# Optimization experiments

Hardware: AMD Instinct MI355X
Metric: run time of the kernel (lower is better)

Reference implementation:

```python
import jax, jax.numpy as jnp
import numpy as np

N = 50000
E = 400000
D = 128

def _linear(v, W, b):
    return v @ W + b

def setup_inputs() -> dict:
    key = jax.random.key(0)
    ks = jax.random.split(key, 24)
    inp = {
        'h': jax.random.normal(ks[0], (N, D), jnp.float32),
        'x': jax.random.normal(ks[1], (N, 3), jnp.float32),
        'src': jax.random.randint(ks[2], (E,), 0, N, jnp.int32),
        'dst': jax.random.randint(ks[3], (E,), 0, N, jnp.int32),
        'distances': jax.random.uniform(ks[4], (E,), jnp.float32),
        'bpp_bias': jax.random.uniform(ks[5], (E,), jnp.float32),
        'msa_bias': jax.random.uniform(ks[6], (E,), jnp.float32),
        'chem_bias': jax.random.uniform(ks[7], (E,), jnp.float32),
        'relative_offset': jax.random.normal(ks[8], (E,), jnp.float32),
        'chain_break_mask': jax.random.uniform(ks[9], (E,), jnp.float32),
    }
    s = 0.05
    # weights stored [in, out] (transpose of torch Linear)
    inp['msg_W1'] = jax.random.normal(ks[10], (2 * D + 6, D), jnp.float32) * s
    inp['msg_b1'] = jnp.zeros((D,), jnp.float32)
    inp['msg_W2'] = jax.random.normal(ks[11], (D, D), jnp.float32) * s
    inp['msg_b2'] = jnp.zeros((D,), jnp.float32)
    inp['h_W1'] = jax.random.normal(ks[12], (2 * D, D), jnp.float32) * s
    inp['h_b1'] = jnp.zeros((D,), jnp.float32)
    inp['h_W2'] = jax.random.normal(ks[13], (D, D), jnp.float32) * s
    inp['h_b2'] = jnp.zeros((D,), jnp.float32)
    inp['c_W1'] = jax.random.normal(ks[14], (D, D), jnp.float32) * s
    inp['c_b1'] = jnp.zeros((D,), jnp.float32)
    inp['c_W2'] = jax.random.normal(ks[15], (D, 1), jnp.float32) * s
    inp['c_b2'] = jnp.zeros((1,), jnp.float32)
    return inp

def reference(h, x, src, dst, distances, bpp_bias, msa_bias, chem_bias,
              relative_offset, chain_break_mask,
              msg_W1, msg_b1, msg_W2, msg_b2,
              h_W1, h_b1, h_W2, h_b2,
              c_W1, c_b1, c_W2, c_b2):
    n = h.shape[0]
    h_src = h[src]                      # [E, D]
    h_dst = h[dst]                      # [E, D]
    diff = x[src] - x[dst]              # [E, 3]
    dist2 = (distances * distances)[:, None]
    feat = jnp.concatenate([
        h_src, h_dst, dist2,
        bpp_bias[:, None], msa_bias[:, None], chem_bias[:, None],
        relative_offset[:, None], chain_break_mask[:, None]], axis=-1)  # [E, 2D+6]
    m_ij = jax.nn.silu(_linear(jax.nn.silu(_linear(feat, msg_W1, msg_b1)), msg_W2, msg_b2))  # [E, D]
    counts = jax.ops.segment_sum(jnp.ones((src.shape[0],), h.dtype), src, num_segments=n)[:, None]  # [N,1]
    denom = jnp.maximum(counts, 1.0)
    m_i = jax.ops.segment_sum(m_ij, src, num_segments=n) / denom      # [N, D]
    h_out = h + _linear(jax.nn.silu(_linear(jnp.concatenate([h, m_i], -1), h_W1, h_b1)), h_W2, h_b2)
    coef = jnp.tanh(_linear(jax.nn.silu(_linear(m_ij, c_W1, c_b1)), c_W2, c_b2))  # [E, 1]
    delta = jax.ops.segment_sum(diff * coef, src, num_segments=n) / denom          # [N, 3]
    x_out = x + delta
    return h_out, x_out
```

## Files before the change

### kernel.cpp

```cpp
#include <hip/hip_runtime.h>
#include <hip/hip_bf16.h>

typedef short bf16x8 __attribute__((ext_vector_type(8)));
typedef float f32x16 __attribute__((ext_vector_type(16)));
typedef int   i32x4v __attribute__((ext_vector_type(4)));
typedef unsigned u32;

#define MFMA32(a,b,c) __builtin_amdgcn_mfma_f32_32x32x16_bf16((a),(b),(c),0,0,0)

__device__ __forceinline__ u32 pkbf(float x, float y) {
  union { u32 u; __hip_bfloat16 h[2]; } t;
  t.h[0] = __float2bfloat16(x);
  t.h[1] = __float2bfloat16(y);
  return t.u;
}
__device__ __forceinline__ float bf2f(u32 lo16) {
  union { u32 u; float f; } t; t.u = lo16 << 16; return t.f;
}
__device__ __forceinline__ float silu_f(float v) { return v / (1.f + __expf(-v)); }
__device__ __forceinline__ float tanh_f(float v) {
  float e = __expf(2.f * fabsf(v));
  float t = 1.f - 2.f / (e + 1.f);
  return copysignf(t, v);
}

template<int NT>
__device__ __forceinline__ void stage_w128t(const float* __restrict__ W, short* wA, int tid) {
  for (int p = tid; p < 8192; p += NT) {
    int j = p & 127;
    int k = (p >> 7) << 1;
    u32 u = pkbf(W[k * 128 + j], W[k * 128 + 128 + j]);
    int off = j * 256 + (((k >> 3) ^ (j & 15)) << 4) + ((k & 7) << 1);
    *(u32*)((char*)wA + off) = u;
  }
}
__device__ __forceinline__ bf16x8 ldsA(const short* wA, int j, int kbase) {
  int off = j * 256 + (((kbase >> 3) ^ (j & 15)) << 4);
  return __builtin_bit_cast(bf16x8, *(const i32x4v*)((const char*)wA + off));
}

__device__ __forceinline__ void row_chunks(u32 p0, u32 p1, u32 p2, u32 p3,
                                           u32 p4, u32 p5, u32 p6, u32 p7,
                                           int hi, char* rowptr, int jm) {
  u32 x0 = (u32)__shfl_xor((int)(hi ? p0 : p4), 32);
  u32 x1 = (u32)__shfl_xor((int)(hi ? p1 : p5), 32);
  u32 x2 = (u32)__shfl_xor((int)(hi ? p2 : p6), 32);
  u32 x3 = (u32)__shfl_xor((int)(hi ? p3 : p7), 32);
  i32x4v c0, c1;
  if (hi) {
    c0[0] = (int)x0; c0[1] = (int)x1; c0[2] = (int)p4; c0[3] = (int)p5;
    c1[0] = (int)x2; c1[1] = (int)x3; c1[2] = (int)p6; c1[3] = (int)p7;
  } else {
    c0[0] = (int)p0; c0[1] = (int)p1; c0[2] = (int)x0; c0[3] = (int)x1;
    c1[0] = (int)p2; c1[1] = (int)p3; c1[2] = (int)x2; c1[3] = (int)x3;
  }
  __builtin_nontemporal_store(c0, (i32x4v*)(rowptr + jm * 64 + hi * 32));
  __builtin_nontemporal_store(c1, (i32x4v*)(rowptr + jm * 64 + hi * 32 + 16));
}

__device__ __forceinline__ void trans_store1(const f32x16& a, const float* bias, int hi,
                                             char* rowptr, bool va, int jm) {
  float v[16];
  #pragma unroll
  for (int r = 0; r < 16; ++r) {
    int rowloc = (r & 3) + 8 * (r >> 2) + 4 * hi;
    v[r] = silu_f(a[r] + bias[jm * 32 + rowloc]);
  }
  u32 p0 = pkbf(v[0], v[1]),  p1 = pkbf(v[2], v[3]);
  u32 p2 = pkbf(v[4], v[5]),  p3 = pkbf(v[6], v[7]);
  u32 p4 = pkbf(v[8], v[9]),  p5 = pkbf(v[10], v[11]);
  u32 p6 = pkbf(v[12], v[13]), p7 = pkbf(v[14], v[15]);
  if (va) row_chunks(p0, p1, p2, p3, p4, p5, p6, p7, hi, rowptr, jm);
}

__device__ __forceinline__ void trans_frag1(const f32x16& a, const float* bias, int hi,
                                            i32x4v* fr, char* rowptr, bool va, int jm) {
  float v[16];
  #pragma unroll
  for (int r = 0; r < 16; ++r) {
    int rowloc = (r & 3) + 8 * (r >> 2) + 4 * hi;
    v[r] = silu_f(a[r] + bias[jm * 32 + rowloc]);
  }
  u32 p0 = pkbf(v[0], v[1]),  p1 = pkbf(v[2], v[3]);
  u32 p2 = pkbf(v[4], v[5]),  p3 = pkbf(v[6], v[7]);
  u32 p4 = pkbf(v[8], v[9]),  p5 = pkbf(v[10], v[11]);
  u32 p6 = pkbf(v[12], v[13]), p7 = pkbf(v[14], v[15]);
  {
    u32 g1 = (u32)__shfl_xor((int)(hi ? p0 : p2), 32);
    u32 g2 = (u32)__shfl_xor((int)(hi ? p1 : p3), 32);
    i32x4v w;
    w[0] = hi ? (int)g1 : (int)p0;
    w[1] = hi ? (int)g2 : (int)p1;
    w[2] = hi ? (int)p2 : (int)g1;
    w[3] = hi ? (int)p3 : (int)g2;
    fr[jm * 2] = w;
    u32 g1b = (u32)__shfl_xor((int)(hi ? p4 : p6), 32);
    u32 g2b = (u32)__shfl_xor((int)(hi ? p5 : p7), 32);
    i32x4v w2;
    w2[0] = hi ? (int)g1b : (int)p4;
    w2[1] = hi ? (int)g2b : (int)p5;
    w2[2] = hi ? (int)p6 : (int)g1b;
    w2[3] = hi ? (int)p7 : (int)g2b;
    fr[jm * 2 + 1] = w2;
  }
  if (va) row_chunks(p0, p1, p2, p3, p4, p5, p6, p7, hi, rowptr, jm);
}


__global__ void kconv(const float* __restrict__ h, char* __restrict__ hbf, int total16) {
  int i = blockIdx.x * 256 + threadIdx.x;
  if (i >= total16) return;
  const float4* h4 = (const float4*)h;
  float4 a = h4[(size_t)i * 2], b = h4[(size_t)i * 2 + 1];
  i32x4v w;
  w[0] = (int)pkbf(a.x, a.y); w[1] = (int)pkbf(a.z, a.w);
  w[2] = (int)pkbf(b.x, b.y); w[3] = (int)pkbf(b.z, b.w);
  *(i32x4v*)(hbf + (size_t)i * 16) = w;
}

__global__ void khist(const int* __restrict__ src, int* __restrict__ cnt, int E) {
  int e = blockIdx.x * 256 + threadIdx.x;
  if (e < E) atomicAdd(&cnt[src[e]], 1);
}

__global__ void kscan1(const int* __restrict__ cnt, int* __restrict__ part,
                       int* __restrict__ bsums, int N) {
  __shared__ int sh[1024];
  int tid = threadIdx.x, i = blockIdx.x * 1024 + tid;
  int v = (i < N) ? cnt[i] : 0;
  sh[tid] = v; __syncthreads();
  for (int off = 1; off < 1024; off <<= 1) {
    int t = (tid >= off) ? sh[tid - off] : 0;
    __syncthreads();
    sh[tid] += t;
    __syncthreads();
  }
  if (i < N) part[i] = sh[tid] - v;
  if (tid == 1023) bsums[blockIdx.x] = sh[1023];
}

__global__ void kscan2(int* __restrict__ bsums, int nb) {
  __shared__ int sh[64];
  int tid = threadIdx.x;
  int v = (tid < nb) ? bsums[tid] : 0;
  sh[tid] = v; __syncthreads();
  for (int off = 1; off < 64; off <<= 1) {
    int t = (tid >= off) ? sh[tid - off] : 0;
    __syncthreads();
    sh[tid] += t;
    __syncthreads();
  }
  if (tid < nb) bsums[tid] = sh[tid] - v;
}

__global__ void kscan3(const int* __restrict__ bsums, int* __restrict__ part,
                       int* __restrict__ head, int N) {
  int i = blockIdx.x * 1024 + threadIdx.x;
  if (i < N) {
    int v = part[i] + bsums[blockIdx.x];
    part[i] = v;
    head[i] = v;
  }
}

__global__ void kscatter(const int* __restrict__ src, const int* __restrict__ dst,
                         const float* __restrict__ dist, const float* __restrict__ bpp,
                         const float* __restrict__ msa, const float* __restrict__ chem,
                         const float* __restrict__ rel, const float* __restrict__ cbm,
                         int* __restrict__ head, int* __restrict__ rec, int E) {
  int e = blockIdx.x * 256 + threadIdx.x;
  if (e >= E) return;
  int s = src[e];
  int p = atomicAdd(&head[s], 1);
  float q = dist[e];
  i32x4v a;
  a[0] = s;
  a[1] = dst[e];
  a[2] = (int)pkbf(q * q, bpp[e]);
  a[3] = (int)pkbf(msa[e], chem[e]);
  *(i32x4v*)(rec + (size_t)p * 8) = a;
  rec[(size_t)p * 8 + 4] = (int)pkbf(rel[e], cbm[e]);
}

__global__ __launch_bounds__(512, 2)
void kedgeA(const char* __restrict__ hbf, const int* __restrict__ rec,
            const float* __restrict__ mW1, const float* __restrict__ mb1,
            char* __restrict__ t1, int E)
{
  __shared__ short wA0[16384], wA1[16384];
  __shared__ short wE[2048];
  __shared__ float sb1[128];

  const int tid = threadIdx.x, wid = tid >> 6, lane = tid & 63;
  const int col = lane & 31, hi = lane >> 5;

  stage_w128t<512>(mW1, wA0, tid);
  stage_w128t<512>(mW1 + 16384, wA1, tid);
  for (int p = tid; p < 2048; p += 512) {
    int j = p >> 4, kk = p & 15;
    float w = (kk < 6) ? mW1[(256 + kk) * 128 + j] : 0.f;
    wE[j * 16 + kk] = (short)(pkbf(w, 0.f) & 0xffffu);
  }
  if (tid < 128) sb1[tid] = mb1[tid];
  __syncthreads();

  const int T = (E + 31) / 32;
  const int stride = gridDim.x * 8;
  int t = blockIdx.x * 8 + wid;
  if (t >= T) return;

  int p = t * 32 + col;
  int pc = p < E ? p : E - 1;
  i32x4v ra = *(const i32x4v*)(rec + (size_t)pc * 8);
  int ev2 = rec[(size_t)pc * 8 + 4];

  while (t < T) {
    bool va = p < E;
    int s = ra[0], d = ra[1];

    i32x4v bs[8], bd[8];
    #pragma unroll
    for (int kc = 0; kc < 8; ++kc)
      bs[kc] = *(const i32x4v*)(hbf + (size_t)s * 256 + kc * 32 + hi * 16);
    #pragma unroll
    for (int kc = 0; kc < 8; ++kc)
      bd[kc] = *(const i32x4v*)(hbf + (size_t)d * 256 + kc * 32 + hi * 16);

    int tn = t + stride;
    int pn = tn * 32 + col;
    int pcn = pn < E ? pn : E - 1;
    i32x4v nra = *(const i32x4v*)(rec + (size_t)pcn * 8);
    int nev2 = rec[(size_t)pcn * 8 + 4];

    char* rowptr = t1 + (size_t)p * 256;
    #pragma unroll
    for (int g = 0; g < 2; ++g) {
      f32x16 acc2[2];
      #pragma unroll
      for (int j2 = 0; j2 < 2; ++j2)
        #pragma unroll
        for (int r = 0; r < 16; ++r) acc2[j2][r] = 0.f;

      #pragma unroll
      for (int kc = 0; kc < 8; ++kc) {
        bf16x8 bb = __builtin_bit_cast(bf16x8, bs[kc]);
        #pragma unroll
        for (int j2 = 0; j2 < 2; ++j2)
          acc2[j2] = MFMA32(ldsA(wA0, (g * 2 + j2) * 32 + col, kc * 16 + hi * 8), bb, acc2[j2]);
      }
      #pragma unroll
      for (int kc = 0; kc < 8; ++kc) {
        bf16x8 bb = __builtin_bit_cast(bf16x8, bd[kc]);
        #pragma unroll
        for (int j2 = 0; j2 < 2; ++j2)
          acc2[j2] = MFMA32(ldsA(wA1, (g * 2 + j2) * 32 + col, kc * 16 + hi * 8), bb, acc2[j2]);
      }
      {
        i32x4v ev;
        ev[0] = hi ? 0 : ra[2];
        ev[1] = hi ? 0 : ra[3];
        ev[2] = hi ? 0 : ev2;
        ev[3] = 0;
        bf16x8 be = __builtin_bit_cast(bf16x8, ev);
        #pragma unroll
        for (int j2 = 0; j2 < 2; ++j2) {
          bf16x8 af = __builtin_bit_cast(bf16x8,
              *(const i32x4v*)((const char*)wE + ((g * 2 + j2) * 32 + col) * 32 + hi * 16));
          acc2[j2] = MFMA32(af, be, acc2[j2]);
        }
      }
      #pragma unroll
      for (int j2 = 0; j2 < 2; ++j2)
        trans_store1(acc2[j2], sb1, hi, rowptr, va, g * 2 + j2);
    }

    t = tn; p = pn; ra = nra; ev2 = nev2;
  }
}

__global__ __launch_bounds__(512, 2)
void kedgeB(char* buf,
            const float* __restrict__ mW2, const float* __restrict__ mb2,
            const float* __restrict__ cW1, const float* __restrict__ cb1,
            const float* __restrict__ cW2v, const float* __restrict__ cb2,
            float* __restrict__ coef, int E)
{
  __shared__ short wA2[16384], wA3[16384];
  __shared__ float sb2[128], scb1[128], scw2[128];
  __shared__ float scb2v[1];

  const int tid = threadIdx.x, wid = tid >> 6, lane = tid & 63;
  const int col = lane & 31, hi = lane >> 5;

  stage_w128t<512>(mW2, wA2, tid);
  stage_w128t<512>(cW1, wA3, tid);
  if (tid < 128) {
    sb2[tid] = mb2[tid]; scb1[tid] = cb1[tid]; scw2[tid] = cW2v[tid];
  }
  if (tid == 0) scb2v[0] = cb2[0];
  __syncthreads();

  const int T = (E + 31) / 32;
  const int stride = gridDim.x * 8;
  for (int t = blockIdx.x * 8 + wid; t < T; t += stride) {
    int p = t * 32 + col;
    bool va = p < E;
    int pc = va ? p : E - 1;

    i32x4v b[8];
    #pragma unroll
    for (int kc = 0; kc < 8; ++kc)
      b[kc] = __builtin_nontemporal_load(
          (const i32x4v*)(buf + (size_t)pc * 256 + kc * 32 + hi * 16));

    char* rowptr = buf + (size_t)p * 256;
    i32x4v fr[8];
    #pragma unroll
    for (int g = 0; g < 2; ++g) {
      f32x16 acc2[2];
      #pragma unroll
      for (int j2 = 0; j2 < 2; ++j2)
        #pragma unroll
        for (int r = 0; r < 16; ++r) acc2[j2][r] = 0.f;
      #pragma unroll
      for (int kc = 0; kc < 8; ++kc) {
        bf16x8 bb = __builtin_bit_cast(bf16x8, b[kc]);
        #pragma unroll
        for (int j2 = 0; j2 < 2; ++j2)
          acc2[j2] = MFMA32(ldsA(wA2, (g * 2 + j2) * 32 + col, kc * 16 + hi * 8), bb, acc2[j2]);
      }
      #pragma unroll
      for (int j2 = 0; j2 < 2; ++j2)
        trans_frag1(acc2[j2], sb2, hi, fr, rowptr, va, g * 2 + j2);
    }

    float part = 0.f;
    #pragma unroll
    for (int g = 0; g < 2; ++g) {
      f32x16 acc2[2];
      #pragma unroll
      for (int j2 = 0; j2 < 2; ++j2)
        #pragma unroll
        for (int r = 0; r < 16; ++r) acc2[j2][r] = 0.f;
      #pragma unroll
      for (int kc = 0; kc < 8; ++kc) {
        bf16x8 bb = __builtin_bit_cast(bf16x8, fr[kc]);
        #pragma unroll
        for (int j2 = 0; j2 < 2; ++j2)
          acc2[j2] = MFMA32(ldsA(wA3, (g * 2 + j2) * 32 + col, kc * 16 + hi * 8), bb, acc2[j2]);
      }
      #pragma unroll
      for (int j2 = 0; j2 < 2; ++j2) {
        int jm = g * 2 + j2;
        #pragma unroll
        for (int r = 0; r < 16; ++r) {
          int rowloc = (r & 3) + 8 * (r >> 2) + 4 * hi;
          part += silu_f(acc2[j2][r] + scb1[jm * 32 + rowloc]) * scw2[jm * 32 + rowloc];
        }
      }
    }
    part += __shfl_xor(part, 32);
    float cf = tanh_f(part + scb2v[0]);
    if (va && hi == 0) coef[p] = cf;
  }
}

__global__ __launch_bounds__(256)
void kagg(const char* __restrict__ m_ij, const int* __restrict__ row_start,
          const int* __restrict__ cnt, char* __restrict__ mibf, int N)
{
  int n = blockIdx.x * 16 + (threadIdx.x >> 4);
  int t = threadIdx.x & 15;
  if (n >= N) return;
  int st = row_start[n], c = cnt[n];
  float a[8] = {0.f, 0.f, 0.f, 0.f, 0.f, 0.f, 0.f, 0.f};
  for (int k = 0; k < c; ++k) {
    i32x4v u = __builtin_nontemporal_load(
        (const i32x4v*)(m_ij + (size_t)(st + k) * 256 + t * 16));
    #pragma unroll
    for (int q = 0; q < 4; ++q) {
      u32 w = (u32)u[q];
      a[q * 2]     += bf2f(w & 0xffffu);
      a[q * 2 + 1] += bf2f(w >> 16);
    }
  }
  float inv = 1.f / fmaxf((float)c, 1.f);
  i32x4v o;
  #pragma unroll
  for (int q = 0; q < 4; ++q) o[q] = (int)pkbf(a[q * 2] * inv, a[q * 2 + 1] * inv);
  *(i32x4v*)(mibf + (size_t)n * 256 + t * 16) = o;
}

__global__ __launch_bounds__(256)
void kaggx(const int* __restrict__ row_start, const int* __restrict__ cnt,
           const float* __restrict__ coef, const int* __restrict__ rec,
           const float* __restrict__ x, float* __restrict__ outX, int N)
{
  int n = blockIdx.x * 256 + threadIdx.x;
  if (n >= N) return;
  int st = row_start[n], c = cnt[n];
  float x0 = x[(size_t)n * 3], x1 = x[(size_t)n * 3 + 1], x2 = x[(size_t)n * 3 + 2];
  float dx = 0.f, dy = 0.f, dz = 0.f;
  for (int k = 0; k < c; ++k) {
    float cf = coef[st + k];
    int dn = rec[(size_t)(st + k) * 8 + 1];
    dx += (x0 - x[(size_t)dn * 3])     * cf;
    dy += (x1 - x[(size_t)dn * 3 + 1]) * cf;
    dz += (x2 - x[(size_t)dn * 3 + 2]) * cf;
  }
  float inv = 1.f / fmaxf((float)c, 1.f);
  outX[(size_t)n * 3]     = x0 + dx * inv;
  outX[(size_t)n * 3 + 1] = x1 + dy * inv;
  outX[(size_t)n * 3 + 2] = x2 + dz * inv;
}

__global__ __launch_bounds__(512, 2)
void knode1(const char* __restrict__ hbf, const char* __restrict__ mibf,
            const float* __restrict__ hW1, const float* __restrict__ hb1,
            char* __restrict__ t1h, int N)
{
  __shared__ short wA0[16384], wA1[16384];
  __shared__ float sb1[128];
  const int tid = threadIdx.x, wid = tid >> 6, lane = tid & 63;
  const int col = lane & 31, hi = lane >> 5;
  stage_w128t<512>(hW1, wA0, tid);
  stage_w128t<512>(hW1 + 16384, wA1, tid);
  if (tid < 128) sb1[tid] = hb1[tid];
  __syncthreads();

  int T = (N + 31) / 32;
  int t = blockIdx.x * 8 + wid;
  if (t >= T) return;
  int n = t * 32 + col;
  bool va = n < N;
  int nc = va ? n : N - 1;

  i32x4v bh[8], bm[8];
  #pragma unroll
  for (int kc = 0; kc < 8; ++kc)
    bh[kc] = *(const i32x4v*)(hbf + (size_t)nc * 256 + kc * 32 + hi * 16);
  #pragma unroll
  for (int kc = 0; kc < 8; ++kc)
    bm[kc] = *(const i32x4v*)(mibf + (size_t)nc * 256 + kc * 32 + hi * 16);

  char* rowptr = t1h + (size_t)n * 256;
  #pragma unroll
  for (int g = 0; g < 2; ++g) {
    f32x16 acc2[2];
    #pragma unroll
    for (int j2 = 0; j2 < 2; ++j2)
      #pragma unroll
      for (int r = 0; r < 16; ++r) acc2[j2][r] = 0.f;
    #pragma unroll
    for (int kc = 0; kc < 8; ++kc) {
      bf16x8 bb = __builtin_bit_cast(bf16x8, bh[kc]);
      #pragma unroll
      for (int j2 = 0; j2 < 2; ++j2)
        acc2[j2] = MFMA32(ldsA(wA0, (g * 2 + j2) * 32 + col, kc * 16 + hi * 8), bb, acc2[j2]);
    }
    #pragma unroll
    for (int kc = 0; kc < 8; ++kc) {
      bf16x8 bb = __builtin_bit_cast(bf16x8, bm[kc]);
      #pragma unroll
      for (int j2 = 0; j2 < 2; ++j2)
        acc2[j2] = MFMA32(ldsA(wA1, (g * 2 + j2) * 32 + col, kc * 16 + hi * 8), bb, acc2[j2]);
    }
    #pragma unroll
    for (int j2 = 0; j2 < 2; ++j2)
      trans_store1(acc2[j2], sb1, hi, rowptr, va, g * 2 + j2);
  }
}

__global__ __launch_bounds__(512, 2)
void knode2(const char* __restrict__ t1h, const float* __restrict__ hW2,
            const float* __restrict__ hb2, const float* __restrict__ h,
            float* __restrict__ outH, int N)
{
  __shared__ short wA0[16384];
  __shared__ float sb2[128];
  const int tid = threadIdx.x, wid = tid >> 6, lane = tid & 63;
  const int col = lane & 31, hi = lane >> 5;
  stage_w128t<512>(hW2, wA0, tid);
  if (tid < 128) sb2[tid] = hb2[tid];
  __syncthreads();

  int T = (N + 31) / 32;
  int t = blockIdx.x * 8 + wid;
  if (t >= T) return;
  int n = t * 32 + col;
  bool va = n < N;
  int nc = va ? n : N - 1;

  i32x4v b[8];
  #pragma unroll
  for (int kc = 0; kc < 8; ++kc)
    b[kc] = __builtin_nontemporal_load(
        (const i32x4v*)(t1h + (size_t)nc * 256 + kc * 32 + hi * 16));

  const float4* h4 = (const float4*)h;
  #pragma unroll
  for (int g = 0; g < 2; ++g) {
    f32x16 acc2[2];
    #pragma unroll
    for (int j2 = 0; j2 < 2; ++j2)
      #pragma unroll
      for (int r = 0; r < 16; ++r) acc2[j2][r] = 0.f;
    #pragma unroll
    for (int kc = 0; kc < 8; ++kc) {
      bf16x8 bb = __builtin_bit_cast(bf16x8, b[kc]);
      #pragma unroll
      for (int j2 = 0; j2 < 2; ++j2)
        acc2[j2] = MFMA32(ldsA(wA0, (g * 2 + j2) * 32 + col, kc * 16 + hi * 8), bb, acc2[j2]);
    }
    #pragma unroll
    for (int j2 = 0; j2 < 2; ++j2) {
      int jm = g * 2 + j2;
      #pragma unroll
      for (int rq = 0; rq < 4; ++rq) {
        int j0 = jm * 32 + rq * 8 + hi * 4;
        float4 hv = h4[(size_t)nc * 32 + (j0 >> 2)];
        float4 o;
        o.x = hv.x + acc2[j2][rq * 4 + 0] + sb2[j0 + 0];
        o.y = hv.y + acc2[j2][rq * 4 + 1] + sb2[j0 + 1];
        o.z = hv.z + acc2[j2][rq * 4 + 2] + sb2[j0 + 2];
        o.w = hv.w + acc2[j2][rq * 4 + 3] + sb2[j0 + 3];
        if (va) ((float4*)outH)[(size_t)nc * 32 + (j0 >> 2)] = o;
      }
    }
  }
}


extern "C" void kernel_launch(void* const* d_in, const int* in_sizes, int n_in,
                              void* d_out, int out_size, void* d_ws, size_t ws_size,
                              hipStream_t stream) {
  const float* h    = (const float*)d_in[0];
  const float* x    = (const float*)d_in[1];
  const int*   src  = (const int*)d_in[2];
  const int*   dst  = (const int*)d_in[3];
  const float* dist = (const float*)d_in[4];
  const float* bpp  = (const float*)d_in[5];
  const float* msa  = (const float*)d_in[6];
  const float* chem = (const float*)d_in[7];
  const float* rel  = (const float*)d_in[8];
  const float* cbm  = (const float*)d_in[9];
  const float* mW1  = (const float*)d_in[10];
  const float* mb1  = (const float*)d_in[11];
  const float* mW2  = (const float*)d_in[12];
  const float* mb2  = (const float*)d_in[13];
  const float* hW1  = (const float*)d_in[14];
  const float* hb1  = (const float*)d_in[15];
  const float* hW2  = (const float*)d_in[16];
  const float* hb2  = (const float*)d_in[17];
  const float* cW1  = (const float*)d_in[18];
  const float* cb1  = (const float*)d_in[19];
  const float* cW2  = (const float*)d_in[20];
  const float* cb2  = (const float*)d_in[21];

  int N = in_sizes[0] / 128;
  int E = in_sizes[2];

  size_t off = 0;
  auto A = [&](size_t b) { size_t o = off; off += (b + 255) & ~(size_t)255; return o; };
  size_t o_cnt  = A((size_t)N * 4);
  size_t o_rs   = A((size_t)N * 4);
  size_t o_head = A((size_t)N * 4);
  size_t o_rec  = A((size_t)E * 32);
  size_t o_coef = A((size_t)E * 4);
  size_t o_bs   = A(1024);
  size_t o_hbf  = A((size_t)N * 256);
  size_t o_mibf = A((size_t)N * 256);
  size_t o_big  = A((size_t)E * 256);

  char* W = (char*)d_ws;
  int*   cnt32 = (int*)(W + o_cnt);
  int*   rs    = (int*)(W + o_rs);
  int*   head  = (int*)(W + o_head);
  int*   rec   = (int*)(W + o_rec);
  float* coef  = (float*)(W + o_coef);
  int*   bsums = (int*)(W + o_bs);
  char*  hbf   = W + o_hbf;
  char*  mibf  = W + o_mibf;
  char*  big   = W + o_big;

  hipMemsetAsync(cnt32, 0, (size_t)N * 4, stream);
  kconv<<<(N * 16 + 255) / 256, 256, 0, stream>>>(h, hbf, N * 16);
  khist<<<(E + 255) / 256, 256, 0, stream>>>(src, cnt32, E);
  int nb = (N + 1023) / 1024;
  kscan1<<<nb, 1024, 0, stream>>>(cnt32, rs, bsums, N);
  kscan2<<<1, 64, 0, stream>>>(bsums, nb);
  kscan3<<<nb, 1024, 0, stream>>>(bsums, rs, head, N);
  kscatter<<<(E + 255) / 256, 256, 0, stream>>>(src, dst, dist, bpp, msa, chem, rel, cbm,
                                                head, rec, E);
  kedgeA<<<512, 512, 0, stream>>>(hbf, rec, mW1, mb1, big, E);
  kedgeB<<<512, 512, 0, stream>>>(big, mW2, mb2, cW1, cb1, cW2, cb2, coef, E);
  kagg<<<(N + 15) / 16, 256, 0, stream>>>(big, rs, cnt32, mibf, N);
  kaggx<<<(N + 255) / 256, 256, 0, stream>>>(rs, cnt32, coef, rec, x,
                                             (float*)d_out + (size_t)N * 128, N);
  int tb = ((N + 31) / 32 + 7) / 8;
  knode1<<<tb, 512, 0, stream>>>(hbf, mibf, hW1, hb1, big, N);
  knode2<<<tb, 512, 0, stream>>>(big, hW2, hb2, h, (float*)d_out, N);
}
```

Measured before the change: 650.0 us.

## Pre-reduce per-source messages within 32-edge tiles inside edge MLP kernel

kedgeB now performs a segmented prefix sum over the 32 edges of each tile, keyed on the source node read from rec, using wave shuffles. Only the tail edge of each segment writes its partial sum back into the message buffer. kagg then reads one partial per 32-edge tile boundary instead of every edge row, which cuts the gather traffic for node aggregation. The cost is 5 shuffle stages over 16 values per fragment in the edge kernel, plus rounding partial sums to bf16.

```diff
diff --git a/kernel.cpp b/kernel.cpp
--- a/kernel.cpp
+++ b/kernel.cpp
@@ -73,37 +73,27 @@
   if (va) row_chunks(p0, p1, p2, p3, p4, p5, p6, p7, hi, rowptr, jm);
 }
 
-__device__ __forceinline__ void trans_frag1(const f32x16& a, const float* bias, int hi,
-                                            i32x4v* fr, char* rowptr, bool va, int jm) {
-  float v[16];
-  #pragma unroll
-  for (int r = 0; r < 16; ++r) {
-    int rowloc = (r & 3) + 8 * (r >> 2) + 4 * hi;
-    v[r] = silu_f(a[r] + bias[jm * 32 + rowloc]);
-  }
+__device__ __forceinline__ void frags_from_v(const float* v, int hi, i32x4v* fr, int jm) {
   u32 p0 = pkbf(v[0], v[1]),  p1 = pkbf(v[2], v[3]);
   u32 p2 = pkbf(v[4], v[5]),  p3 = pkbf(v[6], v[7]);
   u32 p4 = pkbf(v[8], v[9]),  p5 = pkbf(v[10], v[11]);
   u32 p6 = pkbf(v[12], v[13]), p7 = pkbf(v[14], v[15]);
-  {
-    u32 g1 = (u32)__shfl_xor((int)(hi ? p0 : p2), 32);
-    u32 g2 = (u32)__shfl_xor((int)(hi ? p1 : p3), 32);
-    i32x4v w;
-    w[0] = hi ? (int)g1 : (int)p0;
-    w[1] = hi ? (int)g2 : (int)p1;
-    w[2] = hi ? (int)p2 : (int)g1;
-    w[3] = hi ? (int)p3 : (int)g2;
-    fr[jm * 2] = w;
-    u32 g1b = (u32)__shfl_xor((int)(hi ? p4 : p6), 32);
-    u32 g2b = (u32)__shfl_xor((int)(hi ? p5 : p7), 32);
-    i32x4v w2;
-    w2[0] = hi ? (int)g1b : (int)p4;
-    w2[1] = hi ? (int)g2b : (int)p5;
-    w2[2] = hi ? (int)p6 : (int)g1b;
-    w2[3] = hi ? (int)p7 : (int)g2b;
-    fr[jm * 2 + 1] = w2;
-  }
-  if (va) row_chunks(p0, p1, p2, p3, p4, p5, p6, p7, hi, rowptr, jm);
+  u32 g1 = (u32)__shfl_xor((int)(hi ? p0 : p2), 32);
+  u32 g2 = (u32)__shfl_xor((int)(hi ? p1 : p3), 32);
+  i32x4v w;
+  w[0] = hi ? (int)g1 : (int)p0;
+  w[1] = hi ? (int)g2 : (int)p1;
+  w[2] = hi ? (int)p2 : (int)g1;
+  w[3] = hi ? (int)p3 : (int)g2;
+  fr[jm * 2] = w;
+  u32 g1b = (u32)__shfl_xor((int)(hi ? p4 : p6), 32);
+  u32 g2b = (u32)__shfl_xor((int)(hi ? p5 : p7), 32);
+  i32x4v w2;
+  w2[0] = hi ? (int)g1b : (int)p4;
+  w2[1] = hi ? (int)g2b : (int)p5;
+  w2[2] = hi ? (int)p6 : (int)g1b;
+  w2[3] = hi ? (int)p7 : (int)g2b;
+  fr[jm * 2 + 1] = w2;
 }
 
 
@@ -279,7 +269,7 @@
 }
 
 __global__ __launch_bounds__(512, 2)
-void kedgeB(char* buf,
+void kedgeB(char* buf, const int* __restrict__ rec,
             const float* __restrict__ mW2, const float* __restrict__ mb2,
             const float* __restrict__ cW1, const float* __restrict__ cb1,
             const float* __restrict__ cW2v, const float* __restrict__ cb2,
@@ -306,6 +296,7 @@
     int p = t * 32 + col;
     bool va = p < E;
     int pc = va ? p : E - 1;
+    int skey = va ? rec[(size_t)pc * 8] : -1;
 
     i32x4v b[8];
     #pragma unroll
@@ -313,6 +304,18 @@
       b[kc] = __builtin_nontemporal_load(
           (const i32x4v*)(buf + (size_t)pc * 256 + kc * 32 + hi * 16));
 
+    int nk[5];
+    #pragma unroll
+    for (int st = 0; st < 5; ++st) {
+      int off = 1 << st;
+      int sl = (col >= off) ? (lane - off) : lane;
+      nk[st] = __shfl(skey, sl);
+    }
+    int slT = (col == 31) ? lane : (lane + 1);
+    int keyNext = __shfl(skey, slT);
+    bool tail = (col == 31) || (keyNext != skey);
+    bool tv = tail && va;
+
     char* rowptr = buf + (size_t)p * 256;
     i32x4v fr[8];
     #pragma unroll
@@ -330,8 +333,35 @@
           acc2[j2] = MFMA32(ldsA(wA2, (g * 2 + j2) * 32 + col, kc * 16 + hi * 8), bb, acc2[j2]);
       }
       #pragma unroll
-      for (int j2 = 0; j2 < 2; ++j2)
-        trans_frag1(acc2[j2], sb2, hi, fr, rowptr, va, g * 2 + j2);
+      for (int j2 = 0; j2 < 2; ++j2) {
+        int jm = g * 2 + j2;
+        float v[16];
+        #pragma unroll
+        for (int r = 0; r < 16; ++r) {
+          int rowloc = (r & 3) + 8 * (r >> 2) + 4 * hi;
+          v[r] = silu_f(acc2[j2][r] + sb2[jm * 32 + rowloc]);
+        }
+        frags_from_v(v, hi, fr, jm);
+        if (!va)
+          #pragma unroll
+          for (int r = 0; r < 16; ++r) v[r] = 0.f;
+        #pragma unroll
+        for (int st = 0; st < 5; ++st) {
+          int off = 1 << st;
+          int sl = (col >= off) ? (lane - off) : lane;
+          bool ok = (col >= off) && (nk[st] == skey);
+          #pragma unroll
+          for (int r = 0; r < 16; ++r) {
+            float nv = __shfl(v[r], sl);
+            if (ok) v[r] += nv;
+          }
+        }
+        u32 q0 = pkbf(v[0], v[1]),  q1 = pkbf(v[2], v[3]);
+        u32 q2 = pkbf(v[4], v[5]),  q3 = pkbf(v[6], v[7]);
+        u32 q4 = pkbf(v[8], v[9]),  q5 = pkbf(v[10], v[11]);
+        u32 q6 = pkbf(v[12], v[13]), q7 = pkbf(v[14], v[15]);
+        if (tv) row_chunks(q0, q1, q2, q3, q4, q5, q6, q7, hi, rowptr, jm);
+      }
     }
 
     float part = 0.f;
@@ -374,20 +404,34 @@
   if (n >= N) return;
   int st = row_start[n], c = cnt[n];
   float a[8] = {0.f, 0.f, 0.f, 0.f, 0.f, 0.f, 0.f, 0.f};
-  for (int k = 0; k < c; ++k) {
+  if (c > 0) {
+    int last = st + c - 1;
+    int q = st | 31;
+    while (q < last) {
+      i32x4v u = __builtin_nontemporal_load(
+          (const i32x4v*)(m_ij + (size_t)q * 256 + t * 16));
+      #pragma unroll
+      for (int w = 0; w < 4; ++w) {
+        u32 x = (u32)u[w];
+        a[w * 2]     += bf2f(x & 0xffffu);
+        a[w * 2 + 1] += bf2f(x >> 16);
+      }
+      q += 32;
+    }
     i32x4v u = __builtin_nontemporal_load(
-        (const i32x4v*)(m_ij + (size_t)(st + k) * 256 + t * 16));
-    #pragma unroll
-    for (int q = 0; q < 4; ++q) {
-      u32 w = (u32)u[q];
-      a[q * 2]     += bf2f(w & 0xffffu);
-      a[q * 2 + 1] += bf2f(w >> 16);
+        (const i32x4v*)(m_ij + (size_t)last * 256 + t * 16));
+    #pragma unroll
+    for (int w = 0; w < 4; ++w) {
+      u32 x = (u32)u[w];
+      a[w * 2]     += bf2f(x & 0xffffu);
+      a[w * 2 + 1] += bf2f(x >> 16);
     }
   }
   float inv = 1.f / fmaxf((float)c, 1.f);
   i32x4v o;
   #pragma unroll
-  for (int q = 0; q < 4; ++q) o[q] = (int)pkbf(a[q * 2] * inv, a[q * 2 + 1] * inv);
+  for (int q2 = 0; q2 < 4; ++q2)
+    o[q2] = (int)pkbf(a[q2 * 2] * inv, a[q2 * 2 + 1] * inv);
   *(i32x4v*)(mibf + (size_t)n * 256 + t * 16) = o;
 }
 
@@ -593,7 +637,7 @@
   kscatter<<<(E + 255) / 256, 256, 0, stream>>>(src, dst, dist, bpp, msa, chem, rel, cbm,
                                                 head, rec, E);
   kedgeA<<<512, 512, 0, stream>>>(hbf, rec, mW1, mb1, big, E);
-  kedgeB<<<512, 512, 0, stream>>>(big, mW2, mb2, cW1, cb1, cW2, cb2, coef, E);
+  kedgeB<<<512, 512, 0, stream>>>(big, rec, mW2, mb2, cW1, cb1, cW2, cb2, coef, E);
   kagg<<<(N + 15) / 16, 256, 0, stream>>>(big, rs, cnt32, mibf, N);
   kaggx<<<(N + 255) / 256, 256, 0, stream>>>(rs, cnt32, coef, rec, x,
                                              (float*)d_out + (size_t)N * 128, N);
```

Result: slower. 670.4 us (+3.1%).
